# Optimization experiments

Hardware: AMD Instinct MI355X
Metric: run time of the kernel (lower is better)

The kernel has to match this reference:

```python
import jax, jax.numpy as jnp
import numpy as np

D = 512      # model_dim
H = 8        # num_heads
HD = D // H  # head_dim = 64
S = 196      # tokens per channel (14x14 grid)
CHANNELS = np.array([2, 4, 6, 4], dtype=np.int32)  # multiplex channels per sample


def setup_inputs() -> dict:
    key = jax.random.key(0)
    ks = jax.random.split(key, 8)
    C = int(CHANNELS.sum())  # 16
    n = lambda k, shp, s=1.0: jax.random.normal(k, shp, dtype=jnp.float32) * s
    return {
        "x_query": n(ks[0], (C, S, D)),
        "x_keyval": n(ks[1], (C, S, D)),
        "pos": n(ks[2], (C, S, D)),
        "channels": CHANNELS,
        "Wq": n(ks[3], (D, D), 0.02), "bq": jnp.zeros((D,), jnp.float32),
        "Wk": n(ks[4], (D, D), 0.02), "bk": jnp.zeros((D,), jnp.float32),
        "Wv": n(ks[5], (D, D), 0.02), "bv": jnp.zeros((D,), jnp.float32),
        "Wo": n(ks[6], (D, D), 0.02), "bo": jnp.zeros((D,), jnp.float32),
    }


def reference(x_query, x_keyval, pos, channels, Wq, bq, Wk, bk, Wv, bv, Wo, bo):
    C, S_, D_ = x_query.shape
    ch = np.asarray(channels)
    # segment id per packed token; segment i has length channels[i]*S (== cu_seq_len blocks)
    seg = np.repeat(np.arange(ch.shape[0]), ch * S_)                # [T] static
    block_mask = seg[:, None] == seg[None, :]                        # [T,T] static bool

    xq = x_query.reshape(-1, D_)   # [T,D]
    xk = x_keyval.reshape(-1, D_)
    p = pos.reshape(-1, D_)

    # positional embedding fused into Q/K before projection (query_pos/key_pos)
    q = ((xq + p) @ Wq + bq).reshape(-1, H, HD)
    k = ((xk + p) @ Wk + bk).reshape(-1, H, HD)
    v = (xk @ Wv + bv).reshape(-1, H, HD)

    scale = 1.0 / np.sqrt(HD)
    scores = jnp.einsum('qhd,khd->hqk', q, k) * scale               # [H,T,T]
    scores = jnp.where(block_mask[None], scores, jnp.float32(-1e30))
    attn = jax.nn.softmax(scores, axis=-1)
    out = jnp.einsum('hqk,khd->qhd', attn, v).reshape(-1, D_)       # [T,D]
    out = out @ Wo + bo
    return out.reshape(C, S_, D_)
```

## Files before the change

kernel.cpp:

```cpp
#include <hip/hip_runtime.h>
#include <hip/hip_bf16.h>


typedef short short8 __attribute__((ext_vector_type(8)));
typedef float f32x4 __attribute__((ext_vector_type(4)));

__device__ __forceinline__ unsigned short f2b(float f) {
    union { float f; unsigned int i; } x; x.f = f;
    unsigned int r = x.i + 0x7fffu + ((x.i >> 16) & 1u);
    return (unsigned short)(r >> 16);
}

#define NE 1605632
#define WE 262144
#define GS 72
#define LDA 520

__launch_bounds__(256)
__global__ void prep(const float* __restrict__ W0, const float* __restrict__ W1,
                     const float* __restrict__ W2, const float* __restrict__ W3,
                     unsigned short* __restrict__ WF) {
    const int tid = threadIdx.x;
    const float* W = blockIdx.z == 0 ? W0 : blockIdx.z == 1 ? W1 : blockIdx.z == 2 ? W2 : W3;
    unsigned short* T = WF + (size_t)blockIdx.z * WE;
    const int s = blockIdx.x * 4 + (tid >> 6);
    const int f = s >> 4, t = s & 15;
    const int lane = tid & 63, quad = lane >> 4, l16 = lane & 15;
    short8 o;
    #pragma unroll
    for (int j = 0; j < 8; ++j)
        o[j] = (short)f2b(W[(size_t)(t * 32 + quad * 8 + j) * 512 + f * 16 + l16]);
    *(short8*)(T + (size_t)s * 512 + lane * 8) = o;
}

__launch_bounds__(512)
__global__ void qkv_gemm(const float* __restrict__ xq, const float* __restrict__ xk,
                         const float* __restrict__ pos,
                         const unsigned short* __restrict__ WF,
                         const float* __restrict__ bq, const float* __restrict__ bk,
                         const float* __restrict__ bv,
                         unsigned short* __restrict__ qb, unsigned short* __restrict__ kb,
                         unsigned short* __restrict__ vb) {
    __shared__ __align__(16) unsigned short As[32 * LDA];

    const int z = blockIdx.z;
    const float* X = (z == 0) ? xq : xk;
    const bool addp = (z < 2);
    const unsigned short* WFw = WF + (size_t)z * WE;
    const float* bias = (z == 0) ? bq : (z == 1) ? bk : bv;
    unsigned short* C = (z == 0) ? qb : (z == 1) ? kb : vb;

    const int m0 = blockIdx.x * 32;
    const int tid = threadIdx.x;

    #pragma unroll
    for (int p = 0; p < 4; ++p) {
        const int row = p * 8 + (tid >> 6);
        const int col = (tid & 63) * 8;
        const float* src = X + (size_t)(m0 + row) * 512 + col;
        f32x4 a = *(const f32x4*)(src);
        f32x4 b = *(const f32x4*)(src + 4);
        if (addp) {
            const float* ps = pos + (size_t)(m0 + row) * 512 + col;
            f32x4 pa = *(const f32x4*)(ps), pb = *(const f32x4*)(ps + 4);
            #pragma unroll
            for (int j = 0; j < 4; ++j) { a[j] += pa[j]; b[j] += pb[j]; }
        }
        short8 o;
        #pragma unroll
        for (int j = 0; j < 4; ++j) {
            o[j] = (short)f2b(a[j]); o[4 + j] = (short)f2b(b[j]);
        }
        *(short8*)(As + row * LDA + col) = o;
    }
    __syncthreads();

    const int wave = tid >> 6, lane = tid & 63;
    const int quad = lane >> 4, l16 = lane & 15;
    const int n0 = wave * 64;
    const unsigned short* Ar0 = As + l16 * LDA + quad * 8;
    const unsigned short* Bb = WFw + (size_t)lane * 8 + (size_t)n0 * 512;

    f32x4 acc0[4] = {}, acc1[4] = {};
    short8 a0 = *(const short8*)(Ar0);
    short8 a1 = *(const short8*)(Ar0 + 16 * LDA);
    short8 b0 = *(const short8*)(Bb);
    short8 b1 = *(const short8*)(Bb + (size_t)16 * 512);
    short8 b2 = *(const short8*)(Bb + (size_t)32 * 512);
    short8 b3 = *(const short8*)(Bb + (size_t)48 * 512);
    #pragma unroll
    for (int t = 0; t < 16; ++t) {
        short8 na0, na1, nb0, nb1, nb2, nb3;
        if (t < 15) {
            na0 = *(const short8*)(Ar0 + (t + 1) * 32);
            na1 = *(const short8*)(Ar0 + 16 * LDA + (t + 1) * 32);
            nb0 = *(const short8*)(Bb + (size_t)(t + 1) * 512);
            nb1 = *(const short8*)(Bb + (size_t)(16 + t + 1) * 512);
            nb2 = *(const short8*)(Bb + (size_t)(32 + t + 1) * 512);
            nb3 = *(const short8*)(Bb + (size_t)(48 + t + 1) * 512);
        }
        acc0[0] = __builtin_amdgcn_mfma_f32_16x16x32_bf16(a0, b0, acc0[0], 0, 0, 0);
        acc1[0] = __builtin_amdgcn_mfma_f32_16x16x32_bf16(a1, b0, acc1[0], 0, 0, 0);
        acc0[1] = __builtin_amdgcn_mfma_f32_16x16x32_bf16(a0, b1, acc0[1], 0, 0, 0);
        acc1[1] = __builtin_amdgcn_mfma_f32_16x16x32_bf16(a1, b1, acc1[1], 0, 0, 0);
        acc0[2] = __builtin_amdgcn_mfma_f32_16x16x32_bf16(a0, b2, acc0[2], 0, 0, 0);
        acc1[2] = __builtin_amdgcn_mfma_f32_16x16x32_bf16(a1, b2, acc1[2], 0, 0, 0);
        acc0[3] = __builtin_amdgcn_mfma_f32_16x16x32_bf16(a0, b3, acc0[3], 0, 0, 0);
        acc1[3] = __builtin_amdgcn_mfma_f32_16x16x32_bf16(a1, b3, acc1[3], 0, 0, 0);
        a0 = na0; a1 = na1; b0 = nb0; b1 = nb1; b2 = nb2; b3 = nb3;
    }
    #pragma unroll
    for (int nt = 0; nt < 4; ++nt) {
        const int col = n0 + nt * 16 + l16;
        const float bv2 = bias[col];
        #pragma unroll
        for (int r = 0; r < 4; ++r) {
            const int row = m0 + quad * 4 + r;
            C[(size_t)row * 512 + col]        = f2b(acc0[nt][r] + bv2);
            C[(size_t)(row + 16) * 512 + col] = f2b(acc1[nt][r] + bv2);
        }
    }
}

__launch_bounds__(256)
__global__ void out_gemm(const unsigned short* __restrict__ A,
                         const unsigned short* __restrict__ WFo,
                         const float* __restrict__ bo, float* __restrict__ out) {
    const int tid = threadIdx.x;
    const int wave = tid >> 6, lane = tid & 63;
    const int quad = lane >> 4, l16 = lane & 15;
    const int rg = wave & 1, cq = wave >> 1;
    const int m0 = blockIdx.x * 64 + rg * 32;
    const int n0 = blockIdx.y * 128 + cq * 64;
    const unsigned short* Ar0 = A + (size_t)(m0 + l16) * 512 + quad * 8;
    const unsigned short* Bb = WFo + (size_t)lane * 8 + (size_t)n0 * 512;

    f32x4 acc0[4] = {}, acc1[4] = {};
    short8 a0 = *(const short8*)(Ar0);
    short8 a1 = *(const short8*)(Ar0 + 16 * 512);
    short8 b0 = *(const short8*)(Bb);
    short8 b1 = *(const short8*)(Bb + (size_t)16 * 512);
    short8 b2 = *(const short8*)(Bb + (size_t)32 * 512);
    short8 b3 = *(const short8*)(Bb + (size_t)48 * 512);
    #pragma unroll
    for (int t = 0; t < 16; ++t) {
        short8 na0, na1, nb0, nb1, nb2, nb3;
        if (t < 15) {
            na0 = *(const short8*)(Ar0 + (t + 1) * 32);
            na1 = *(const short8*)(Ar0 + 16 * 512 + (t + 1) * 32);
            nb0 = *(const short8*)(Bb + (size_t)(t + 1) * 512);
            nb1 = *(const short8*)(Bb + (size_t)(16 + t + 1) * 512);
            nb2 = *(const short8*)(Bb + (size_t)(32 + t + 1) * 512);
            nb3 = *(const short8*)(Bb + (size_t)(48 + t + 1) * 512);
        }
        acc0[0] = __builtin_amdgcn_mfma_f32_16x16x32_bf16(a0, b0, acc0[0], 0, 0, 0);
        acc1[0] = __builtin_amdgcn_mfma_f32_16x16x32_bf16(a1, b0, acc1[0], 0, 0, 0);
        acc0[1] = __builtin_amdgcn_mfma_f32_16x16x32_bf16(a0, b1, acc0[1], 0, 0, 0);
        acc1[1] = __builtin_amdgcn_mfma_f32_16x16x32_bf16(a1, b1, acc1[1], 0, 0, 0);
        acc0[2] = __builtin_amdgcn_mfma_f32_16x16x32_bf16(a0, b2, acc0[2], 0, 0, 0);
        acc1[2] = __builtin_amdgcn_mfma_f32_16x16x32_bf16(a1, b2, acc1[2], 0, 0, 0);
        acc0[3] = __builtin_amdgcn_mfma_f32_16x16x32_bf16(a0, b3, acc0[3], 0, 0, 0);
        acc1[3] = __builtin_amdgcn_mfma_f32_16x16x32_bf16(a1, b3, acc1[3], 0, 0, 0);
        a0 = na0; a1 = na1; b0 = nb0; b1 = nb1; b2 = nb2; b3 = nb3;
    }
    #pragma unroll
    for (int nt = 0; nt < 4; ++nt) {
        const int col = n0 + nt * 16 + l16;
        const float bv = bo[col];
        #pragma unroll
        for (int r = 0; r < 4; ++r) {
            const int row = m0 + quad * 4 + r;
            out[(size_t)row * 512 + col]        = acc0[nt][r] + bv;
            out[(size_t)(row + 16) * 512 + col] = acc1[nt][r] + bv;
        }
    }
}

__launch_bounds__(512)
__global__ void attn_seg(const unsigned short* __restrict__ q,
                         const unsigned short* __restrict__ k,
                         const unsigned short* __restrict__ v,
                         unsigned short* __restrict__ o) {
    __shared__ __align__(16) unsigned char Lds[55296];

    const int id = blockIdx.x;
    int h, off, L, qt;
    if (id < 152)      { h = id & 7; qt = id >> 3; off = 1176; L = 1176; }
    else if (id < 360) { int m = id - 152; h = m & 7; int s = m >> 3;
                         if (s < 13) { off = 392;  L = 784; qt = s; }
                         else        { off = 2352; L = 784; qt = s - 13; } }
    else               { int m = id - 360; h = m & 7; qt = m >> 3; off = 0; L = 392; }

    const int tid = threadIdx.x;
    const int wave = tid >> 6, lane = tid & 63;
    const int grp = wave >> 2, w4 = wave & 3;
    const int quad = lane >> 4, l16 = lane & 15;
    const int hb = h * 64;
    const int lastr = off + L - 1;

    unsigned short* Ks = (unsigned short*)(Lds + grp * 18432);
    unsigned short* Vt = (unsigned short*)(Lds + grp * 18432 + 9216);
    unsigned char*  Pme = Lds + 36864 + wave * 2304;

    int qrow = off + qt * 64 + w4 * 16 + l16;
    if (qrow > lastr) qrow = lastr;
    const short8 qf0 = *(const short8*)(q + (size_t)qrow * 512 + hb + quad * 8);
    const short8 qf1 = *(const short8*)(q + (size_t)qrow * 512 + hb + 32 + quad * 8);

    const int skey = lane, sd = w4 * 16;
    const int ntiles = (L + 63) >> 6;
    const int nt0 = (ntiles + 1) >> 1;

    float lsum = 0.f;
    f32x4 oacc[4] = {};

    short8 kr0, kr1, vr0, vr1;
    {
        int kk = (grp ? nt0 : 0) * 64 + skey;
        int krow = off + (kk < L ? kk : L - 1);
        kr0 = *(const short8*)(k + (size_t)krow * 512 + hb + sd);
        kr1 = *(const short8*)(k + (size_t)krow * 512 + hb + sd + 8);
        vr0 = *(const short8*)(v + (size_t)krow * 512 + hb + sd);
        vr1 = *(const short8*)(v + (size_t)krow * 512 + hb + sd + 8);
    }
    unsigned char* pwr = Pme + l16 * 144 + quad * 8;
    const unsigned char* prd = Pme + l16 * 144 + quad * 16;

    for (int i = 0; i < nt0; ++i) {
        const int tg = (grp ? nt0 : 0) + i;
        __syncthreads();
        *(short8*)(Ks + skey * GS + sd)     = kr0;
        *(short8*)(Ks + skey * GS + sd + 8) = kr1;
        #pragma unroll
        for (int j = 0; j < 8; ++j) {
            Vt[(sd + j) * GS + skey]     = (unsigned short)vr0[j];
            Vt[(sd + 8 + j) * GS + skey] = (unsigned short)vr1[j];
        }
        __syncthreads();
        if (i + 1 < nt0) {
            int kk = (tg + 1) * 64 + skey;
            int krow = off + (kk < L ? kk : L - 1);
            kr0 = *(const short8*)(k + (size_t)krow * 512 + hb + sd);
            kr1 = *(const short8*)(k + (size_t)krow * 512 + hb + sd + 8);
            vr0 = *(const short8*)(v + (size_t)krow * 512 + hb + sd);
            vr1 = *(const short8*)(v + (size_t)krow * 512 + hb + sd + 8);
        }
        f32x4 sT[4];
        __builtin_amdgcn_s_setprio(1);
        #pragma unroll
        for (int g = 0; g < 4; ++g) {
            short8 kb0 = *(const short8*)(Ks + (g * 16 + l16) * GS + quad * 8);
            short8 kb1 = *(const short8*)(Ks + (g * 16 + l16) * GS + 32 + quad * 8);
            f32x4 z = {0.f, 0.f, 0.f, 0.f};
            z     = __builtin_amdgcn_mfma_f32_16x16x32_bf16(kb0, qf0, z, 0, 0, 0);
            sT[g] = __builtin_amdgcn_mfma_f32_16x16x32_bf16(kb1, qf1, z, 0, 0, 0);
        }
        __builtin_amdgcn_s_setprio(0);
        const int kbase = tg * 64 + quad * 4;
        #pragma unroll
        for (int g = 0; g < 4; ++g) {
            float p[4];
            #pragma unroll
            for (int r = 0; r < 4; ++r) {
                const bool valid = (kbase + g * 16 + r) < L;
                p[r] = valid ? __expf(fminf(sT[g][r] * 0.125f, 30.f)) : 0.f;
                lsum += p[r];
            }
            #pragma unroll
            for (int i2 = 0; i2 < 2; ++i2) {
                __hip_bfloat162 t = __float22bfloat162_rn(make_float2(p[2 * i2], p[2 * i2 + 1]));
                *(unsigned int*)(pwr + g * 32 + i2 * 4) = *(unsigned int*)&t;
            }
        }
        short8 pa0 = *(const short8*)(prd);
        short8 pa1 = *(const short8*)(prd + 64);
        __builtin_amdgcn_s_setprio(1);
        #pragma unroll
        for (int nt = 0; nt < 4; ++nt) {
            short8 vf0 = *(const short8*)(Vt + (nt * 16 + l16) * GS + quad * 8);
            short8 vf1 = *(const short8*)(Vt + (nt * 16 + l16) * GS + 32 + quad * 8);
            oacc[nt] = __builtin_amdgcn_mfma_f32_16x16x32_bf16(pa0, vf0, oacc[nt], 0, 0, 0);
            oacc[nt] = __builtin_amdgcn_mfma_f32_16x16x32_bf16(pa1, vf1, oacc[nt], 0, 0, 0);
        }
        __builtin_amdgcn_s_setprio(0);
    }
    lsum += __shfl_xor(lsum, 16);
    lsum += __shfl_xor(lsum, 32);

    __syncthreads();
    float* Mrg = (float*)(Lds + w4 * 5120 + lane * 80);
    float* Ls  = (float*)(Lds + 20480);
    if (grp == 1) {
        #pragma unroll
        for (int nt = 0; nt < 4; ++nt) *(f32x4*)(Mrg + nt * 4) = oacc[nt];
        Ls[w4 * 64 + lane] = lsum;
    }
    __syncthreads();
    if (grp == 0) {
        lsum += Ls[w4 * 64 + lane];
        #pragma unroll
        for (int nt = 0; nt < 4; ++nt) {
            f32x4 po = *(const f32x4*)(Mrg + nt * 4);
            oacc[nt] += po;
        }
        #pragma unroll
        for (int r = 0; r < 4; ++r) {
            const float srow = __shfl(lsum, (lane & 48) + quad * 4 + r);
            const float linv = 1.0f / srow;
            const int qi = qt * 64 + w4 * 16 + quad * 4 + r;
            if (qi < L) {
                #pragma unroll
                for (int nt = 0; nt < 4; ++nt)
                    o[(size_t)(off + qi) * 512 + hb + nt * 16 + l16] = f2b(oacc[nt][r] * linv);
            }
        }
    }
}

extern "C" void kernel_launch(void* const* d_in, const int* in_sizes, int n_in,
                              void* d_out, int out_size, void* d_ws, size_t ws_size,
                              hipStream_t stream) {
    const float* xq  = (const float*)d_in[0];
    const float* xk  = (const float*)d_in[1];
    const float* pos = (const float*)d_in[2];
    const float* Wq = (const float*)d_in[4];
    const float* bq = (const float*)d_in[5];
    const float* Wk = (const float*)d_in[6];
    const float* bk = (const float*)d_in[7];
    const float* Wv = (const float*)d_in[8];
    const float* bv = (const float*)d_in[9];
    const float* Wo = (const float*)d_in[10];
    const float* bo = (const float*)d_in[11];
    float* out = (float*)d_out;

    unsigned short* ws = (unsigned short*)d_ws;
    unsigned short* qb = ws;
    unsigned short* kb = ws + NE;
    unsigned short* vb = ws + (size_t)2 * NE;
    unsigned short* WF = ws + (size_t)3 * NE;

    prep<<<dim3(128, 1, 4), 256, 0, stream>>>(Wq, Wk, Wv, Wo, WF);
    qkv_gemm<<<dim3(98, 1, 3), 512, 0, stream>>>(xq, xk, pos, WF, bq, bk, bv,
                                                 qb, kb, vb);
    attn_seg<<<dim3(416), 512, 0, stream>>>(qb, kb, vb, qb);
    out_gemm<<<dim3(49, 4), 256, 0, stream>>>(qb, WF + (size_t)3 * WE, bo, out);
}
```

Measured before the change: 135.1 us.

## Emit V projection transposed so attention loads V^T with vector LDS stores

The QKV projection kernel now writes the V output in a transposed [D][T] layout with 4-element vector stores. The attention kernel reads each head-dim row of V^T directly and writes it to LDS with two 16-byte stores. This replaces the per-element scalar transpose writes into shared memory. In exchange, the global V loads are now strided per lane, the projection's stores are column-scattered, and tail chunks rely on clamping to L-8, which is valid only because the segment lengths are multiples of 8.

```diff
diff --git a/kernel.cpp b/kernel.cpp
--- a/kernel.cpp
+++ b/kernel.cpp
@@ -4,6 +4,7 @@
 
 typedef short short8 __attribute__((ext_vector_type(8)));
 typedef float f32x4 __attribute__((ext_vector_type(4)));
+typedef unsigned short ushort4v __attribute__((ext_vector_type(4)));
 
 __device__ __forceinline__ unsigned short f2b(float f) {
     union { float f; unsigned int i; } x; x.f = f;
@@ -15,6 +16,7 @@
 #define WE 262144
 #define GS 72
 #define LDA 520
+#define TT 3136
 
 __launch_bounds__(256)
 __global__ void prep(const float* __restrict__ W0, const float* __restrict__ W1,
@@ -109,15 +111,31 @@
         acc1[3] = __builtin_amdgcn_mfma_f32_16x16x32_bf16(a1, b3, acc1[3], 0, 0, 0);
         a0 = na0; a1 = na1; b0 = nb0; b1 = nb1; b2 = nb2; b3 = nb3;
     }
-    #pragma unroll
-    for (int nt = 0; nt < 4; ++nt) {
-        const int col = n0 + nt * 16 + l16;
-        const float bv2 = bias[col];
-        #pragma unroll
-        for (int r = 0; r < 4; ++r) {
-            const int row = m0 + quad * 4 + r;
-            C[(size_t)row * 512 + col]        = f2b(acc0[nt][r] + bv2);
-            C[(size_t)(row + 16) * 512 + col] = f2b(acc1[nt][r] + bv2);
+    if (z == 2) {
+        #pragma unroll
+        for (int nt = 0; nt < 4; ++nt) {
+            const int col = n0 + nt * 16 + l16;
+            const float bv2 = bias[col];
+            ushort4v w0, w1;
+            #pragma unroll
+            for (int r = 0; r < 4; ++r) {
+                w0[r] = f2b(acc0[nt][r] + bv2);
+                w1[r] = f2b(acc1[nt][r] + bv2);
+            }
+            *(ushort4v*)(C + (size_t)col * TT + m0 + quad * 4)      = w0;
+            *(ushort4v*)(C + (size_t)col * TT + m0 + 16 + quad * 4) = w1;
+        }
+    } else {
+        #pragma unroll
+        for (int nt = 0; nt < 4; ++nt) {
+            const int col = n0 + nt * 16 + l16;
+            const float bv2 = bias[col];
+            #pragma unroll
+            for (int r = 0; r < 4; ++r) {
+                const int row = m0 + quad * 4 + r;
+                C[(size_t)row * 512 + col]        = f2b(acc0[nt][r] + bv2);
+                C[(size_t)(row + 16) * 512 + col] = f2b(acc1[nt][r] + bv2);
+            }
         }
     }
 }
@@ -179,7 +197,7 @@
 __launch_bounds__(512)
 __global__ void attn_seg(const unsigned short* __restrict__ q,
                          const unsigned short* __restrict__ k,
-                         const unsigned short* __restrict__ v,
+                         const unsigned short* __restrict__ vt,
                          unsigned short* __restrict__ o) {
     __shared__ __align__(16) unsigned char Lds[55296];
 
@@ -208,20 +226,24 @@
     const short8 qf1 = *(const short8*)(q + (size_t)qrow * 512 + hb + 32 + quad * 8);
 
     const int skey = lane, sd = w4 * 16;
+    const unsigned short* vrow = vt + (size_t)(hb + lane) * TT + off;
     const int ntiles = (L + 63) >> 6;
     const int nt0 = (ntiles + 1) >> 1;
 
     float lsum = 0.f;
     f32x4 oacc[4] = {};
 
-    short8 kr0, kr1, vr0, vr1;
+    short8 kr0, kr1, vs0, vs1;
     {
-        int kk = (grp ? nt0 : 0) * 64 + skey;
+        const int tb = (grp ? nt0 : 0) * 64;
+        int kk = tb + skey;
         int krow = off + (kk < L ? kk : L - 1);
         kr0 = *(const short8*)(k + (size_t)krow * 512 + hb + sd);
         kr1 = *(const short8*)(k + (size_t)krow * 512 + hb + sd + 8);
-        vr0 = *(const short8*)(v + (size_t)krow * 512 + hb + sd);
-        vr1 = *(const short8*)(v + (size_t)krow * 512 + hb + sd + 8);
+        int c0 = tb + w4 * 16;     if (c0 + 8 > L) c0 = L - 8;
+        int c1 = tb + w4 * 16 + 8; if (c1 + 8 > L) c1 = L - 8;
+        vs0 = *(const short8*)(vrow + c0);
+        vs1 = *(const short8*)(vrow + c1);
     }
     unsigned char* pwr = Pme + l16 * 144 + quad * 8;
     const unsigned char* prd = Pme + l16 * 144 + quad * 16;
@@ -231,19 +253,19 @@
         __syncthreads();
         *(short8*)(Ks + skey * GS + sd)     = kr0;
         *(short8*)(Ks + skey * GS + sd + 8) = kr1;
-        #pragma unroll
-        for (int j = 0; j < 8; ++j) {
-            Vt[(sd + j) * GS + skey]     = (unsigned short)vr0[j];
-            Vt[(sd + 8 + j) * GS + skey] = (unsigned short)vr1[j];
-        }
+        *(short8*)(Vt + lane * GS + w4 * 16)     = vs0;
+        *(short8*)(Vt + lane * GS + w4 * 16 + 8) = vs1;
         __syncthreads();
         if (i + 1 < nt0) {
-            int kk = (tg + 1) * 64 + skey;
+            const int tb = (tg + 1) * 64;
+            int kk = tb + skey;
             int krow = off + (kk < L ? kk : L - 1);
             kr0 = *(const short8*)(k + (size_t)krow * 512 + hb + sd);
             kr1 = *(const short8*)(k + (size_t)krow * 512 + hb + sd + 8);
-            vr0 = *(const short8*)(v + (size_t)krow * 512 + hb + sd);
-            vr1 = *(const short8*)(v + (size_t)krow * 512 + hb + sd + 8);
+            int c0 = tb + w4 * 16;     if (c0 + 8 > L) c0 = L - 8;
+            int c1 = tb + w4 * 16 + 8; if (c1 + 8 > L) c1 = L - 8;
+            vs0 = *(const short8*)(vrow + c0);
+            vs1 = *(const short8*)(vrow + c1);
         }
         f32x4 sT[4];
         __builtin_amdgcn_s_setprio(1);
```

Result: no change. 135.1 us, median of 2 (-0.0%).
